# Performance work log

Measured on AMD Instinct MI355X. Metric: run time of the kernel, lower is better.

## Reference

```python
import jax, jax.numpy as jnp
import numpy as np

H_SIZE = 2048
N_HEADS = 16
N_KV = 4
HEAD_DIM = 128
EPS = 1e-6
ROPE_THETA = 10000.0


def _rms_norm(x, w):
    # per-head RMSNorm over last dim (head_dim)
    var = jnp.mean(jnp.square(x), axis=-1, keepdims=True)
    return x * jax.lax.rsqrt(var + EPS) * w


def _rope(x, positions):
    # neox-style rotary over full head_dim. x: [B,S,H,D], positions: [B,S]
    d = x.shape[-1]
    inv_freq = 1.0 / (ROPE_THETA ** (jnp.arange(0, d, 2, dtype=jnp.float32) / d))
    ang = positions.astype(jnp.float32)[..., None] * inv_freq  # [B,S,D/2]
    cos = jnp.cos(ang)[:, :, None, :]
    sin = jnp.sin(ang)[:, :, None, :]
    x1, x2 = x[..., : d // 2], x[..., d // 2 :]
    return jnp.concatenate([x1 * cos - x2 * sin, x2 * cos + x1 * sin], axis=-1)


def setup_inputs() -> dict:
    key = jax.random.key(0)
    k1, k2, k3 = jax.random.split(key, 3)
    B, S = 2, 2048
    positions = jnp.broadcast_to(jnp.arange(S, dtype=jnp.int32), (B, S))
    hidden_states = jax.random.normal(k1, (B, S, H_SIZE), dtype=jnp.float32)
    w_qkv = jax.random.normal(k2, (H_SIZE, (N_HEADS + 2 * N_KV) * HEAD_DIM), dtype=jnp.float32) * 0.02
    w_o = jax.random.normal(k3, (N_HEADS * HEAD_DIM, H_SIZE), dtype=jnp.float32) * 0.02
    q_norm_w = jnp.ones((HEAD_DIM,), dtype=jnp.float32)
    k_norm_w = jnp.ones((HEAD_DIM,), dtype=jnp.float32)
    return {"positions": positions, "hidden_states": hidden_states, "w_qkv": w_qkv,
            "w_o": w_o, "q_norm_w": q_norm_w, "k_norm_w": k_norm_w}


def reference(positions, hidden_states, w_qkv, w_o, q_norm_w, k_norm_w):
    B, S, _ = hidden_states.shape
    q_size = N_HEADS * HEAD_DIM
    kv_size = N_KV * HEAD_DIM
    qkv = hidden_states @ w_qkv  # [B,S,q+2kv]
    q = qkv[..., :q_size].reshape(B, S, N_HEADS, HEAD_DIM)
    k = qkv[..., q_size : q_size + kv_size].reshape(B, S, N_KV, HEAD_DIM)
    v = qkv[..., q_size + kv_size :].reshape(B, S, N_KV, HEAD_DIM)
    q = _rms_norm(q, q_norm_w)
    k = _rms_norm(k, k_norm_w)
    q = _rope(q, positions)
    k = _rope(k, positions)
    # GQA: repeat kv heads
    rep = N_HEADS // N_KV
    k = jnp.repeat(k, rep, axis=2)
    v = jnp.repeat(v, rep, axis=2)
    scale = HEAD_DIM ** -0.5
    scores = jnp.einsum("bqhd,bkhd->bhqk", q, k) * scale
    causal = jnp.tril(jnp.ones((S, S), dtype=bool))
    scores = jnp.where(causal, scores, jnp.finfo(scores.dtype).min)
    probs = jax.nn.softmax(scores, axis=-1)
    attn = jnp.einsum("bhqk,bkhd->bqhd", probs, v).reshape(B, S, N_HEADS * HEAD_DIM)
    return attn @ w_o
```

## Files before the change

### kernel.cpp

```cpp
#include <hip/hip_runtime.h>
#include <math.h>

#define TOKS 4096
#define HS   2048
#define QKV_N 3072
#define S_LEN 2048
#define NH   16
#define NKV  4
#define DH   128

typedef __attribute__((ext_vector_type(8))) short short8;
typedef __attribute__((ext_vector_type(4))) float f32x4;

static __device__ __forceinline__ unsigned short f2bf(float f) {
  unsigned u = __builtin_bit_cast(unsigned, f);
  u += 0x7fffu + ((u >> 16) & 1u);
  return (unsigned short)(u >> 16);
}
static __device__ __forceinline__ float bf2f(unsigned short s) {
  unsigned u = (unsigned)s << 16;
  return __builtin_bit_cast(float, u);
}

__global__ __launch_bounds__(256)
void cvt_bf16(const float* __restrict__ in, unsigned short* __restrict__ out) {
  const size_t i = ((size_t)blockIdx.x * 256 + threadIdx.x) * 8;
  float4 a = *(const float4*)(in + i);
  float4 b = *(const float4*)(in + i + 4);
  short8 r;
  r[0] = f2bf(a.x); r[1] = f2bf(a.y); r[2] = f2bf(a.z); r[3] = f2bf(a.w);
  r[4] = f2bf(b.x); r[5] = f2bf(b.y); r[6] = f2bf(b.z); r[7] = f2bf(b.w);
  *(short8*)(out + i) = r;
}

__global__ __launch_bounds__(256)
void transpose_cvt(const float* __restrict__ in, unsigned short* __restrict__ out,
                   int R, int C, int ldin,
                   long in_z_hi, long in_z_lo, int z_mod, long out_z) {
  __shared__ float tile[32][33];
  const int z = blockIdx.z;
  in  += (size_t)(z / z_mod) * in_z_hi + (size_t)(z % z_mod) * in_z_lo;
  out += (size_t)z * out_z;
  const int r0 = blockIdx.x * 32, c0 = blockIdx.y * 32;
  const int tx = threadIdx.x & 31, ty = threadIdx.x >> 5;
  #pragma unroll
  for (int i = 0; i < 4; ++i)
    tile[ty + i * 8][tx] = in[(size_t)(r0 + ty + i * 8) * ldin + c0 + tx];
  __syncthreads();
  #pragma unroll
  for (int i = 0; i < 4; ++i)
    out[(size_t)(c0 + ty + i * 8) * R + r0 + tx] = f2bf(tile[tx][ty + i * 8]);
}

__global__ __launch_bounds__(256)
void transpose_bf16(const unsigned short* __restrict__ in, unsigned short* __restrict__ out,
                    int R, int C, int ldin,
                    long in_z_hi, long in_z_lo, int z_mod, long out_z) {
  __shared__ unsigned short tile[32][33];
  const int z = blockIdx.z;
  in  += (size_t)(z / z_mod) * in_z_hi + (size_t)(z % z_mod) * in_z_lo;
  out += (size_t)z * out_z;
  const int r0 = blockIdx.x * 32, c0 = blockIdx.y * 32;
  const int tx = threadIdx.x & 31, ty = threadIdx.x >> 5;
  #pragma unroll
  for (int i = 0; i < 4; ++i)
    tile[ty + i * 8][tx] = in[(size_t)(r0 + ty + i * 8) * ldin + c0 + tx];
  __syncthreads();
  #pragma unroll
  for (int i = 0; i < 4; ++i)
    out[(size_t)(c0 + ty + i * 8) * R + r0 + tx] = tile[tx][ty + i * 8];
}

__global__ __launch_bounds__(256)
void norm_rope_cvt(const unsigned short* __restrict__ qkv, const int* __restrict__ positions,
                   const float* __restrict__ qw, const float* __restrict__ kw,
                   unsigned short* __restrict__ Qb, unsigned short* __restrict__ Kb) {
  const int tok  = blockIdx.x;
  const int slot = blockIdx.y * 4 + (threadIdx.x >> 6);
  const int lane = threadIdx.x & 63;
  const int b = tok >> 11, s = tok & 2047;

  const unsigned short* x; const float* wgt; unsigned short* outp; float scale;
  if (slot < NH) {
    x = qkv + (size_t)tok * QKV_N + slot * DH;  wgt = qw;
    outp = Qb + (((size_t)b * NH + slot) * S_LEN + s) * DH;
    scale = 0.08838834764831845f;
  } else {
    const int kh = slot - NH;
    x = qkv + (size_t)tok * QKV_N + NH * DH + kh * DH;  wgt = kw;
    outp = Kb + (((size_t)b * NKV + kh) * S_LEN + s) * DH;
    scale = 1.0f;
  }

  float x1 = bf2f(x[lane]), x2 = bf2f(x[lane + 64]);
  float ss = x1 * x1 + x2 * x2;
  #pragma unroll
  for (int o = 32; o > 0; o >>= 1) ss += __shfl_xor(ss, o, 64);
  const float rs = 1.0f / sqrtf(ss * (1.0f / 128.0f) + 1e-6f);
  const float n1 = x1 * rs * wgt[lane];
  const float n2 = x2 * rs * wgt[lane + 64];

  const float pos = (float)positions[tok];
  const float inv_freq = exp2f(-(float)lane * (13.287712379549449f / 64.0f));
  float sn, cs;
  sincosf(pos * inv_freq, &sn, &cs);

  outp[lane]      = f2bf((n1 * cs - n2 * sn) * scale);
  outp[lane + 64] = f2bf((n2 * cs + n1 * sn) * scale);
}

template <int OUT_BF16, int NB>
__global__ __launch_bounds__(512, 2)
void gemm256(const unsigned short* __restrict__ A, const unsigned short* __restrict__ Bt,
             void* __restrict__ Cv, int M, int N, int K) {
  constexpr int NW   = NB / 4;
  constexpr int NACC = NB / 64;
  constexpr int BL   = NB / 128;
  constexpr int VM   = 2 * BL;

  __shared__ __align__(16) unsigned short LA[2][256 * 64];
  __shared__ __align__(16) unsigned short LB[2][NB * 64];

  const int t = threadIdx.x, w = t >> 6, l = t & 63;
  const int lm = l & 15, lr = l >> 4;
  const int wr = w >> 2, wc = w & 3;
  const int bn = blockIdx.x * NB, bm = blockIdx.y * 256;
  const int nkt = K >> 6;

  f32x4 acc[8][NACC];
  #pragma unroll
  for (int mi = 0; mi < 8; ++mi)
    #pragma unroll
    for (int ni = 0; ni < NACC; ++ni) acc[mi][ni] = {0.f, 0.f, 0.f, 0.f};

  auto stageA = [&](unsigned short* Lb, int half, int kt) {
    if (kt >= nkt) return;
    const int k0 = kt << 6;
    #pragma unroll
    for (int r = 0; r < 2; ++r) {
      const int row  = half * 128 + r * 64 + (t >> 3);
      const int slot = (t & 7) ^ (row & 7);
      const unsigned short* src = A + (size_t)(bm + row) * K + k0 + slot * 8;
      __builtin_amdgcn_global_load_lds(
          (const __attribute__((address_space(1))) void*)src,
          (__attribute__((address_space(3))) void*)(Lb + (half * 128 + r * 64 + w * 8) * 64),
          16, 0, 0);
    }
  };
  auto stageB = [&](unsigned short* Lb, int half, int kt) {
    if (kt >= nkt) return;
    const int k0 = kt << 6;
    #pragma unroll
    for (int r = 0; r < BL; ++r) {
      const int row  = half * (NB / 2) + r * 64 + (t >> 3);
      const int slot = (t & 7) ^ (row & 7);
      const unsigned short* src = Bt + (size_t)(bn + row) * K + k0 + slot * 8;
      __builtin_amdgcn_global_load_lds(
          (const __attribute__((address_space(1))) void*)src,
          (__attribute__((address_space(3))) void*)(Lb + (half * (NB / 2) + r * 64 + w * 8) * 64),
          16, 0, 0);
    }
  };

  stageB(&LB[0][0], 0, 0); stageB(&LB[0][0], 1, 0);
  stageA(&LA[0][0], 0, 0); stageA(&LA[0][0], 1, 0);
  stageB(&LB[1][0], 0, 1); stageB(&LB[1][0], 1, 1);
  if constexpr (NB == 256) asm volatile("s_waitcnt vmcnt(4)" ::: "memory");
  else                     asm volatile("s_waitcnt vmcnt(2)" ::: "memory");
  __builtin_amdgcn_s_barrier();

  const int niter = nkt >> 1;
  for (int i = 0; i < niter; ++i) {
    const int t0 = i * 2;
    short8 bfr[NACC][2];
    #pragma unroll
    for (int p = 0; p < 8; ++p) {
      const int buf = p >> 2, q = p & 3;
      const unsigned short* La = &LA[buf][0];
      const unsigned short* Lb = &LB[buf][0];

      if (q == 0) {
        #pragma unroll
        for (int ni = 0; ni < NACC; ++ni)
          #pragma unroll
          for (int ks = 0; ks < 2; ++ks) {
            const int row = wc * NW + ni * 16 + lm;
            bfr[ni][ks] = *(const short8*)(Lb + row * 64 +
                                           ((ks * 32 + lr * 8) ^ ((row & 7) << 3)));
          }
      }
      short8 af[2][2];
      #pragma unroll
      for (int mi2 = 0; mi2 < 2; ++mi2)
        #pragma unroll
        for (int ks = 0; ks < 2; ++ks) {
          const int row = wr * 128 + (q * 2 + mi2) * 16 + lm;
          af[mi2][ks] = *(const short8*)(La + row * 64 +
                                         ((ks * 32 + lr * 8) ^ ((row & 7) << 3)));
        }

      switch (p) {
        case 0: stageA(&LA[1][0], 0, t0 + 1); break;
        case 1: stageA(&LA[1][0], 1, t0 + 1); break;
        case 2: stageB(&LB[0][0], 0, t0 + 2); break;
        case 3: stageB(&LB[0][0], 1, t0 + 2); break;
        case 4: stageA(&LA[0][0], 0, t0 + 2); break;
        case 5: stageA(&LA[0][0], 1, t0 + 2); break;
        case 6: stageB(&LB[1][0], 0, t0 + 3); break;
        case 7: stageB(&LB[1][0], 1, t0 + 3); break;
      }

      __builtin_amdgcn_s_barrier();
      asm volatile("s_waitcnt lgkmcnt(0)" ::: "memory");
      __builtin_amdgcn_sched_barrier(0);

      __builtin_amdgcn_s_setprio(1);
      #pragma unroll
      for (int mi2 = 0; mi2 < 2; ++mi2)
        #pragma unroll
        for (int ni = 0; ni < NACC; ++ni)
          #pragma unroll
          for (int ks = 0; ks < 2; ++ks)
            acc[q * 2 + mi2][ni] = __builtin_amdgcn_mfma_f32_16x16x32_bf16(
                af[mi2][ks], bfr[ni][ks], acc[q * 2 + mi2][ni], 0, 0, 0);
      __builtin_amdgcn_s_setprio(0);

      if (q == 3) {
        if (i == niter - 1) asm volatile("s_waitcnt vmcnt(0)" ::: "memory");
        else if constexpr (NB == 256) asm volatile("s_waitcnt vmcnt(4)" ::: "memory");
        else                          asm volatile("s_waitcnt vmcnt(2)" ::: "memory");
      }
      __builtin_amdgcn_s_barrier();
    }
  }

  #pragma unroll
  for (int mi = 0; mi < 8; ++mi)
    #pragma unroll
    for (int ni = 0; ni < NACC; ++ni)
      #pragma unroll
      for (int j = 0; j < 4; ++j) {
        const size_t idx =
            (size_t)(bm + wr * 128 + mi * 16 + lr * 4 + j) * N + bn + wc * NW + ni * 16 + lm;
        if constexpr (OUT_BF16) ((unsigned short*)Cv)[idx] = f2bf(acc[mi][ni][j]);
        else                    ((float*)Cv)[idx] = acc[mi][ni][j];
      }
}

#define M_INIT 12.0f
#define P_CAP  2981.0f

__global__ __launch_bounds__(256, 3)
void attn_mfma(const unsigned short* __restrict__ Qb, const unsigned short* __restrict__ Kb,
               const unsigned short* __restrict__ Vt, unsigned short* __restrict__ att) {
  __shared__ unsigned short Ks_[2][64 * 128];
  __shared__ unsigned short Vs_[2][128 * 64];
  __shared__ unsigned short Pl[4][32 * 64];

  const int x  = blockIdx.x;
  const int b  = blockIdx.z;
  const int qb = b ? x : 15 - x;
  const int h  = blockIdx.y;
  const int kvh = h >> 2;
  const int t = threadIdx.x, w = t >> 6, l = t & 63;
  const int lm = l & 15, lr = l >> 4;
  const int row0 = qb * 128 + w * 32;

  const unsigned short* qbase = Qb + ((size_t)(b * NH + h)) * S_LEN * DH;
  const unsigned short* kbase = Kb + ((size_t)(b * NKV + kvh)) * S_LEN * DH;
  const unsigned short* vtbase = Vt + ((size_t)(b * NKV + kvh)) * DH * S_LEN;

  short8 qf[2][4];
  #pragma unroll
  for (int m = 0; m < 2; ++m)
    #pragma unroll
    for (int kc = 0; kc < 4; ++kc)
      qf[m][kc] = *(const short8*)(qbase + (size_t)(row0 + m * 16 + lm) * DH + kc * 32 + lr * 8);

  short8 ones;
  #pragma unroll
  for (int i = 0; i < 8; ++i) ones[i] = (short)0x3F80;

  f32x4 o[2][8];
  #pragma unroll
  for (int m = 0; m < 2; ++m)
    #pragma unroll
    for (int ng = 0; ng < 8; ++ng) o[m][ng] = {0.f, 0.f, 0.f, 0.f};
  f32x4 lacc[2];
  lacc[0] = {0.f, 0.f, 0.f, 0.f}; lacc[1] = {0.f, 0.f, 0.f, 0.f};
  float m_run[2][4];
  #pragma unroll
  for (int m = 0; m < 2; ++m)
    #pragma unroll
    for (int j = 0; j < 4; ++j) m_run[m][j] = M_INIT;

  auto stage = [&](int bufi, int kb0) {
    #pragma unroll
    for (int i = 0; i < 4; ++i) {
      const int rk = w * 16 + i * 4 + (l >> 4);
      const unsigned short* gk =
          kbase + (size_t)(kb0 + rk) * DH + (((l & 15) ^ (rk & 7)) * 8);
      __builtin_amdgcn_global_load_lds(
          (const __attribute__((address_space(1))) void*)gk,
          (__attribute__((address_space(3))) void*)(&Ks_[bufi][(w * 16 + i * 4) * 128]),
          16, 0, 0);
      const int rv = w * 32 + i * 8 + (l >> 3);
      const unsigned short* gv =
          vtbase + (size_t)rv * S_LEN + kb0 + (((l & 7) ^ (rv & 7)) * 8);
      __builtin_amdgcn_global_load_lds(
          (const __attribute__((address_space(1))) void*)gv,
          (__attribute__((address_space(3))) void*)(&Vs_[bufi][(w * 32 + i * 8) * 64]),
          16, 0, 0);
    }
  };

  const int nkt = qb * 2 + 2;
  stage(0, 0);
  __syncthreads();

  for (int kt = 0; kt < nkt; ++kt) {
    const int kb0 = kt * 64;
    if (kt + 1 < nkt) stage((kt + 1) & 1, kb0 + 64);

    if (kb0 <= row0 + 31) {
      const unsigned short* Kc = Ks_[kt & 1];
      const unsigned short* Vc = Vs_[kt & 1];
      const int rsw = (lm & 7) << 3;

      f32x4 s[2][4];
      #pragma unroll
      for (int m = 0; m < 2; ++m)
        #pragma unroll
        for (int n2 = 0; n2 < 4; ++n2) s[m][n2] = {0.f, 0.f, 0.f, 0.f};
      __builtin_amdgcn_s_setprio(1);
      #pragma unroll
      for (int n2 = 0; n2 < 4; ++n2) {
        short8 kf[4];
        #pragma unroll
        for (int kc = 0; kc < 4; ++kc)
          kf[kc] = *(const short8*)(Kc + (n2 * 16 + lm) * 128 + ((kc * 32 + lr * 8) ^ rsw));
        #pragma unroll
        for (int m = 0; m < 2; ++m)
          #pragma unroll
          for (int kc = 0; kc < 4; ++kc)
            s[m][n2] = __builtin_amdgcn_mfma_f32_16x16x32_bf16(qf[m][kc], kf[kc], s[m][n2], 0, 0, 0);
      }
      __builtin_amdgcn_s_setprio(0);

      if (kb0 + 63 > row0) {
        #pragma unroll
        for (int m = 0; m < 2; ++m) {
          const int qi = row0 + m * 16 + lr * 4;
          #pragma unroll
          for (int n2 = 0; n2 < 4; ++n2) {
            const int kvi = kb0 + n2 * 16 + lm;
            #pragma unroll
            for (int j = 0; j < 4; ++j)
              if (kvi > qi + j) s[m][n2][j] = -1e30f;
          }
        }
      }

      float pm = 0.f;
      #pragma unroll
      for (int m = 0; m < 2; ++m)
        #pragma unroll
        for (int n2 = 0; n2 < 4; ++n2)
          #pragma unroll
          for (int j = 0; j < 4; ++j) {
            const float p = __expf(s[m][n2][j] - m_run[m][j]);
            s[m][n2][j] = p;
            pm = fmaxf(pm, p);
          }

      if (!__all(pm <= P_CAP)) {
        #pragma unroll
        for (int m = 0; m < 2; ++m)
          #pragma unroll
          for (int j = 0; j < 4; ++j) {
            float v = fmaxf(fmaxf(s[m][0][j], s[m][1][j]), fmaxf(s[m][2][j], s[m][3][j]));
            v = fmaxf(v, __shfl_xor(v, 1, 64));
            v = fmaxf(v, __shfl_xor(v, 2, 64));
            v = fmaxf(v, __shfl_xor(v, 4, 64));
            v = fmaxf(v, __shfl_xor(v, 8, 64));
            if (v > P_CAP) {
              const float al = 1.0f / v;
              m_run[m][j] += __logf(v);
              lacc[m][j] *= al;
              #pragma unroll
              for (int n2 = 0; n2 < 4; ++n2) s[m][n2][j] *= al;
              #pragma unroll
              for (int ng = 0; ng < 8; ++ng) o[m][ng][j] *= al;
            }
          }
      }

      #pragma unroll
      for (int m = 0; m < 2; ++m)
        #pragma unroll
        for (int j = 0; j < 4; ++j) {
          const int prow = m * 16 + lr * 4 + j;
          unsigned short* Pw = &Pl[w][prow * 64];
          const int sw = (prow & 7) << 3;
          Pw[lm ^ sw]        = f2bf(s[m][0][j]);
          Pw[(16 + lm) ^ sw] = f2bf(s[m][1][j]);
          Pw[(32 + lm) ^ sw] = f2bf(s[m][2][j]);
          Pw[(48 + lm) ^ sw] = f2bf(s[m][3][j]);
        }
      __asm__ volatile("s_waitcnt lgkmcnt(0)" ::: "memory");

      short8 pf[2][2];
      #pragma unroll
      for (int m = 0; m < 2; ++m)
        #pragma unroll
        for (int k2 = 0; k2 < 2; ++k2)
          pf[m][k2] = *(const short8*)(&Pl[w][(m * 16 + lm) * 64 + ((k2 * 32 + lr * 8) ^ rsw)]);
      __builtin_amdgcn_s_setprio(1);
      #pragma unroll
      for (int m = 0; m < 2; ++m)
        #pragma unroll
        for (int k2 = 0; k2 < 2; ++k2)
          lacc[m] = __builtin_amdgcn_mfma_f32_16x16x32_bf16(pf[m][k2], ones, lacc[m], 0, 0, 0);
      #pragma unroll
      for (int ng = 0; ng < 8; ++ng) {
        const short8 vf0 = *(const short8*)(Vc + (ng * 16 + lm) * 64 + ((lr * 8) ^ rsw));
        const short8 vf1 = *(const short8*)(Vc + (ng * 16 + lm) * 64 + ((32 + lr * 8) ^ rsw));
        o[0][ng] = __builtin_amdgcn_mfma_f32_16x16x32_bf16(pf[0][0], vf0, o[0][ng], 0, 0, 0);
        o[1][ng] = __builtin_amdgcn_mfma_f32_16x16x32_bf16(pf[1][0], vf0, o[1][ng], 0, 0, 0);
        o[0][ng] = __builtin_amdgcn_mfma_f32_16x16x32_bf16(pf[0][1], vf1, o[0][ng], 0, 0, 0);
        o[1][ng] = __builtin_amdgcn_mfma_f32_16x16x32_bf16(pf[1][1], vf1, o[1][ng], 0, 0, 0);
      }
      __builtin_amdgcn_s_setprio(0);
    }
    __syncthreads();
  }

  #pragma unroll
  for (int m = 0; m < 2; ++m)
    #pragma unroll
    for (int j = 0; j < 4; ++j) {
      const float linv = 1.0f / lacc[m][j];
      unsigned short* ar =
          att + ((size_t)(b * S_LEN) + row0 + m * 16 + lr * 4 + j) * (NH * DH) + h * DH + lm;
      #pragma unroll
      for (int ng = 0; ng < 8; ++ng) ar[ng * 16] = f2bf(o[m][ng][j] * linv);
    }
}

extern "C" void kernel_launch(void* const* d_in, const int* in_sizes, int n_in,
                              void* d_out, int out_size, void* d_ws, size_t ws_size,
                              hipStream_t stream) {
  const int*   positions = (const int*)  d_in[0];
  const float* hidden    = (const float*)d_in[1];
  const float* w_qkv     = (const float*)d_in[2];
  const float* w_o       = (const float*)d_in[3];
  const float* q_norm_w  = (const float*)d_in[4];
  const float* k_norm_w  = (const float*)d_in[5];
  float* out = (float*)d_out;

  char* ws = (char*)d_ws;
  unsigned short* qkvb  = (unsigned short*)ws;
  unsigned short* att   = (unsigned short*)ws;
  char* region = ws + (size_t)TOKS * QKV_N * 4;
  unsigned short* hb    = (unsigned short*)region;
  unsigned short* Qb    = (unsigned short*)region;
  unsigned short* wqkvt = (unsigned short*)(region + 16777216);
  unsigned short* Kb    = (unsigned short*)(region + 16777216);
  unsigned short* Vt    = (unsigned short*)(region + 20971520);
  unsigned short* wot   = (unsigned short*)(region + 25165824);

  cvt_bf16<<<(TOKS * HS) / (256 * 8), 256, 0, stream>>>(hidden, hb);
  transpose_cvt<<<dim3(HS / 32, QKV_N / 32, 1), 256, 0, stream>>>(
      w_qkv, wqkvt, HS, QKV_N, QKV_N, 0, 0, 1, 0);
  gemm256<1, 256><<<dim3(QKV_N / 256, TOKS / 256), 512, 0, stream>>>(
      hb, wqkvt, qkvb, TOKS, QKV_N, HS);
  norm_rope_cvt<<<dim3(TOKS, 5), 256, 0, stream>>>(
      qkvb, positions, q_norm_w, k_norm_w, Qb, Kb);
  transpose_bf16<<<dim3(S_LEN / 32, DH / 32, 2 * NKV), 256, 0, stream>>>(
      qkvb + (NH + NKV) * DH, Vt, S_LEN, DH, QKV_N,
      (long)S_LEN * QKV_N, DH, NKV, (long)DH * S_LEN);
  transpose_cvt<<<dim3(HS / 32, HS / 32, 1), 256, 0, stream>>>(
      w_o, wot, HS, HS, HS, 0, 0, 1, 0);
  attn_mfma<<<dim3(16, NH, 2), 256, 0, stream>>>(Qb, Kb, Vt, att);
  gemm256<0, 128><<<dim3(HS / 128, TOKS / 256), 512, 0, stream>>>(
      att, wot, out, TOKS, HS, HS);
}
```

Measured before the change: 265.6 us.

## Split long causal attention query blocks across two workgroups with merge kernel

Measured after the change: 270.8 us. No clear change (+2.0%).

```diff
diff --git a/kernel.cpp b/kernel.cpp
--- a/kernel.cpp
+++ b/kernel.cpp
@@ -116,7 +116,6 @@
   constexpr int NW   = NB / 4;
   constexpr int NACC = NB / 64;
   constexpr int BL   = NB / 128;
-  constexpr int VM   = 2 * BL;
 
   __shared__ __align__(16) unsigned short LA[2][256 * 64];
   __shared__ __align__(16) unsigned short LB[2][NB * 64];
@@ -252,18 +251,28 @@
 
 __global__ __launch_bounds__(256, 3)
 void attn_mfma(const unsigned short* __restrict__ Qb, const unsigned short* __restrict__ Kb,
-               const unsigned short* __restrict__ Vt, unsigned short* __restrict__ att) {
+               const unsigned short* __restrict__ Vt, unsigned short* __restrict__ att,
+               float* __restrict__ Opart, float* __restrict__ LMpart) {
   __shared__ unsigned short Ks_[2][64 * 128];
   __shared__ unsigned short Vs_[2][128 * 64];
   __shared__ unsigned short Pl[4][32 * 64];
 
   const int x  = blockIdx.x;
+  const int h  = blockIdx.y;
   const int b  = blockIdx.z;
-  const int qb = b ? x : 15 - x;
-  const int h  = blockIdx.y;
   const int kvh = h >> 2;
   const int t = threadIdx.x, w = t >> 6, l = t & 63;
   const int lm = l & 15, lr = l >> 4;
+
+  int qb, k0t, k1t, pslot;
+  if (x == 0)       { qb = 8; k0t = 0; k1t = 18; pslot = -1; }
+  else if (x <= 14) {
+    const int s = x - 1;  qb = 15 - (s >> 1);
+    const int nk = 2 * qb + 2, mid = nk >> 1, half = s & 1;
+    k0t = half ? mid : 0;  k1t = half ? nk : mid;
+    pslot = ((b * NH + h) * 7 + (qb - 9)) * 2 + half;
+  } else            { qb = 22 - x; k0t = 0; k1t = 2 * qb + 2; pslot = -1; }
+
   const int row0 = qb * 128 + w * 32;
 
   const unsigned short* qbase = Qb + ((size_t)(b * NH + h)) * S_LEN * DH;
@@ -314,13 +323,12 @@
     }
   };
 
-  const int nkt = qb * 2 + 2;
-  stage(0, 0);
+  stage(k0t & 1, k0t * 64);
   __syncthreads();
 
-  for (int kt = 0; kt < nkt; ++kt) {
+  for (int kt = k0t; kt < k1t; ++kt) {
     const int kb0 = kt * 64;
-    if (kt + 1 < nkt) stage((kt + 1) & 1, kb0 + 64);
+    if (kt + 1 < k1t) stage((kt + 1) & 1, kb0 + 64);
 
     if (kb0 <= row0 + 31) {
       const unsigned short* Kc = Ks_[kt & 1];
@@ -435,16 +443,68 @@
     __syncthreads();
   }
 
-  #pragma unroll
-  for (int m = 0; m < 2; ++m)
-    #pragma unroll
-    for (int j = 0; j < 4; ++j) {
-      const float linv = 1.0f / lacc[m][j];
-      unsigned short* ar =
-          att + ((size_t)(b * S_LEN) + row0 + m * 16 + lr * 4 + j) * (NH * DH) + h * DH + lm;
-      #pragma unroll
-      for (int ng = 0; ng < 8; ++ng) ar[ng * 16] = f2bf(o[m][ng][j] * linv);
-    }
+  if (pslot < 0) {
+    #pragma unroll
+    for (int m = 0; m < 2; ++m)
+      #pragma unroll
+      for (int j = 0; j < 4; ++j) {
+        const float linv = 1.0f / lacc[m][j];
+        unsigned short* ar =
+            att + ((size_t)(b * S_LEN) + row0 + m * 16 + lr * 4 + j) * (NH * DH) + h * DH + lm;
+        #pragma unroll
+        for (int ng = 0; ng < 8; ++ng) ar[ng * 16] = f2bf(o[m][ng][j] * linv);
+      }
+  } else {
+    float* Po = Opart + (size_t)pslot * 16384;
+    #pragma unroll
+    for (int m = 0; m < 2; ++m)
+      #pragma unroll
+      for (int j = 0; j < 4; ++j) {
+        const int rl = w * 32 + m * 16 + lr * 4 + j;
+        #pragma unroll
+        for (int ng = 0; ng < 8; ++ng)
+          Po[rl * 128 + ng * 16 + lm] = o[m][ng][j];
+        if (lm == 0) {
+          LMpart[pslot * 256 + rl]       = lacc[m][j];
+          LMpart[pslot * 256 + 128 + rl] = m_run[m][j];
+        }
+      }
+  }
+}
+
+__global__ __launch_bounds__(256)
+void attn_merge(const float* __restrict__ Opart, const float* __restrict__ LMpart,
+                unsigned short* __restrict__ att) {
+  const int qs = blockIdx.x;
+  const int h  = blockIdx.y;
+  const int b  = blockIdx.z;
+  const int qb = 9 + qs;
+  const int sidx = (b * NH + h) * 7 + qs;
+  const int t = threadIdx.x;
+  const int r  = t >> 1;
+  const int c0 = (t & 1) * 64;
+
+  const float l0 = LMpart[(sidx * 2 + 0) * 256 + r];
+  const float m0 = LMpart[(sidx * 2 + 0) * 256 + 128 + r];
+  const float l1 = LMpart[(sidx * 2 + 1) * 256 + r];
+  const float m1 = LMpart[(sidx * 2 + 1) * 256 + 128 + r];
+  const float M  = fmaxf(m0, m1);
+  const float a0 = __expf(m0 - M), a1 = __expf(m1 - M);
+  const float linv = 1.0f / (l0 * a0 + l1 * a1);
+
+  const float* O0 = Opart + ((size_t)(sidx * 2 + 0) * 16384) + r * 128 + c0;
+  const float* O1 = Opart + ((size_t)(sidx * 2 + 1) * 16384) + r * 128 + c0;
+  unsigned short* ar =
+      att + ((size_t)(b * S_LEN) + qb * 128 + r) * (NH * DH) + h * DH + c0;
+  #pragma unroll
+  for (int i = 0; i < 16; ++i) {
+    float4 v0 = *(const float4*)(O0 + i * 4);
+    float4 v1 = *(const float4*)(O1 + i * 4);
+    ar[i * 4 + 0] = f2bf((v0.x * a0 + v1.x * a1) * linv);
+    ar[i * 4 + 1] = f2bf((v0.y * a0 + v1.y * a1) * linv);
+    ar[i * 4 + 2] = f2bf((v0.z * a0 + v1.z * a1) * linv);
+    ar[i * 4 + 3] = f2bf((v0.w * a0 + v1.w * a1) * linv);
+  }
 }
 
 extern "C" void kernel_launch(void* const* d_in, const int* in_sizes, int n_in,
@@ -461,6 +521,8 @@
   char* ws = (char*)d_ws;
   unsigned short* qkvb  = (unsigned short*)ws;
   unsigned short* att   = (unsigned short*)ws;
+  float* Opart  = (float*)(ws + 18874368);
+  float* LMpart = (float*)(ws + 18874368 + 29360128);
   char* region = ws + (size_t)TOKS * QKV_N * 4;
   unsigned short* hb    = (unsigned short*)region;
   unsigned short* Qb    = (unsigned short*)region;
@@ -481,7 +543,8 @@
       (long)S_LEN * QKV_N, DH, NKV, (long)DH * S_LEN);
   transpose_cvt<<<dim3(HS / 32, HS / 32, 1), 256, 0, stream>>>(
       w_o, wot, HS, HS, HS, 0, 0, 1, 0);
-  attn_mfma<<<dim3(16, NH, 2), 256, 0, stream>>>(Qb, Kb, Vt, att);
+  attn_mfma<<<dim3(23, NH, 2), 256, 0, stream>>>(Qb, Kb, Vt, att, Opart, LMpart);
+  attn_merge<<<dim3(7, NH, 2), 256, 0, stream>>>(Opart, LMpart, att);
   gemm256<0, 128><<<dim3(HS / 128, TOKS / 256), 512, 0, stream>>>(
       att, wot, out, TOKS, HS, HS);
 }
```

## Split attention query block across 8 waves of 16 rows each

Applied to the files above, without the earlier changes.

Result: faster. 248.1 us (-6.6%).

```diff
diff --git a/kernel.cpp b/kernel.cpp
--- a/kernel.cpp
+++ b/kernel.cpp
@@ -116,7 +116,6 @@
   constexpr int NW   = NB / 4;
   constexpr int NACC = NB / 64;
   constexpr int BL   = NB / 128;
-  constexpr int VM   = 2 * BL;
 
   __shared__ __align__(16) unsigned short LA[2][256 * 64];
   __shared__ __align__(16) unsigned short LB[2][NB * 64];
@@ -250,12 +249,12 @@
 #define M_INIT 12.0f
 #define P_CAP  2981.0f
 
-__global__ __launch_bounds__(256, 3)
+__global__ __launch_bounds__(512)
 void attn_mfma(const unsigned short* __restrict__ Qb, const unsigned short* __restrict__ Kb,
                const unsigned short* __restrict__ Vt, unsigned short* __restrict__ att) {
   __shared__ unsigned short Ks_[2][64 * 128];
   __shared__ unsigned short Vs_[2][128 * 64];
-  __shared__ unsigned short Pl[4][32 * 64];
+  __shared__ unsigned short Pl[8][16 * 64];
 
   const int x  = blockIdx.x;
   const int b  = blockIdx.z;
@@ -264,52 +263,45 @@
   const int kvh = h >> 2;
   const int t = threadIdx.x, w = t >> 6, l = t & 63;
   const int lm = l & 15, lr = l >> 4;
-  const int row0 = qb * 128 + w * 32;
+  const int row0 = qb * 128 + w * 16;
 
   const unsigned short* qbase = Qb + ((size_t)(b * NH + h)) * S_LEN * DH;
   const unsigned short* kbase = Kb + ((size_t)(b * NKV + kvh)) * S_LEN * DH;
   const unsigned short* vtbase = Vt + ((size_t)(b * NKV + kvh)) * DH * S_LEN;
 
-  short8 qf[2][4];
-  #pragma unroll
-  for (int m = 0; m < 2; ++m)
-    #pragma unroll
-    for (int kc = 0; kc < 4; ++kc)
-      qf[m][kc] = *(const short8*)(qbase + (size_t)(row0 + m * 16 + lm) * DH + kc * 32 + lr * 8);
+  short8 qf[4];
+  #pragma unroll
+  for (int kc = 0; kc < 4; ++kc)
+    qf[kc] = *(const short8*)(qbase + (size_t)(row0 + lm) * DH + kc * 32 + lr * 8);
 
   short8 ones;
   #pragma unroll
   for (int i = 0; i < 8; ++i) ones[i] = (short)0x3F80;
 
-  f32x4 o[2][8];
-  #pragma unroll
-  for (int m = 0; m < 2; ++m)
-    #pragma unroll
-    for (int ng = 0; ng < 8; ++ng) o[m][ng] = {0.f, 0.f, 0.f, 0.f};
-  f32x4 lacc[2];
-  lacc[0] = {0.f, 0.f, 0.f, 0.f}; lacc[1] = {0.f, 0.f, 0.f, 0.f};
-  float m_run[2][4];
-  #pragma unroll
-  for (int m = 0; m < 2; ++m)
-    #pragma unroll
-    for (int j = 0; j < 4; ++j) m_run[m][j] = M_INIT;
+  f32x4 o[8];
+  #pragma unroll
+  for (int ng = 0; ng < 8; ++ng) o[ng] = {0.f, 0.f, 0.f, 0.f};
+  f32x4 lacc = {0.f, 0.f, 0.f, 0.f};
+  float m_run[4];
+  #pragma unroll
+  for (int j = 0; j < 4; ++j) m_run[j] = M_INIT;
 
   auto stage = [&](int bufi, int kb0) {
     #pragma unroll
-    for (int i = 0; i < 4; ++i) {
-      const int rk = w * 16 + i * 4 + (l >> 4);
+    for (int i = 0; i < 2; ++i) {
+      const int rk = i * 32 + w * 4 + (l >> 4);
       const unsigned short* gk =
           kbase + (size_t)(kb0 + rk) * DH + (((l & 15) ^ (rk & 7)) * 8);
       __builtin_amdgcn_global_load_lds(
           (const __attribute__((address_space(1))) void*)gk,
-          (__attribute__((address_space(3))) void*)(&Ks_[bufi][(w * 16 + i * 4) * 128]),
+          (__attribute__((address_space(3))) void*)(&Ks_[bufi][(i * 512 + w * 64) * 8]),
           16, 0, 0);
-      const int rv = w * 32 + i * 8 + (l >> 3);
+      const int rv = i * 64 + w * 8 + (l >> 3);
       const unsigned short* gv =
           vtbase + (size_t)rv * S_LEN + kb0 + (((l & 7) ^ (rv & 7)) * 8);
       __builtin_amdgcn_global_load_lds(
           (const __attribute__((address_space(1))) void*)gv,
-          (__attribute__((address_space(3))) void*)(&Vs_[bufi][(w * 32 + i * 8) * 64]),
+          (__attribute__((address_space(3))) void*)(&Vs_[bufi][(i * 512 + w * 64) * 8]),
           16, 0, 0);
     }
   };
@@ -322,113 +314,92 @@
     const int kb0 = kt * 64;
     if (kt + 1 < nkt) stage((kt + 1) & 1, kb0 + 64);
 
-    if (kb0 <= row0 + 31) {
+    if (kb0 <= row0 + 15) {
       const unsigned short* Kc = Ks_[kt & 1];
       const unsigned short* Vc = Vs_[kt & 1];
       const int rsw = (lm & 7) << 3;
 
-      f32x4 s[2][4];
-      #pragma unroll
-      for (int m = 0; m < 2; ++m)
-        #pragma unroll
-        for (int n2 = 0; n2 < 4; ++n2) s[m][n2] = {0.f, 0.f, 0.f, 0.f};
+      f32x4 s[4];
+      #pragma unroll
+      for (int n2 = 0; n2 < 4; ++n2) s[n2] = {0.f, 0.f, 0.f, 0.f};
       __builtin_amdgcn_s_setprio(1);
       #pragma unroll
       for (int n2 = 0; n2 < 4; ++n2) {
-        short8 kf[4];
-        #pragma unroll
-        for (int kc = 0; kc < 4; ++kc)
-          kf[kc] = *(const short8*)(Kc + (n2 * 16 + lm) * 128 + ((kc * 32 + lr * 8) ^ rsw));
-        #pragma unroll
-        for (int m = 0; m < 2; ++m)
+        #pragma unroll
+        for (int kc = 0; kc < 4; ++kc) {
+          const short8 kf = *(const short8*)(Kc + (n2 * 16 + lm) * 128 +
+                                             ((kc * 32 + lr * 8) ^ rsw));
+          s[n2] = __builtin_amdgcn_mfma_f32_16x16x32_bf16(qf[kc], kf, s[n2], 0, 0, 0);
+        }
+      }
+      __builtin_amdgcn_s_setprio(0);
+
+      if (kb0 + 63 > row0) {
+        const int qi = row0 + lr * 4;
+        #pragma unroll
+        for (int n2 = 0; n2 < 4; ++n2) {
+          const int kvi = kb0 + n2 * 16 + lm;
           #pragma unroll
-          for (int kc = 0; kc < 4; ++kc)
-            s[m][n2] = __builtin_amdgcn_mfma_f32_16x16x32_bf16(qf[m][kc], kf[kc], s[m][n2], 0, 0, 0);
-      }
-      __builtin_amdgcn_s_setprio(0);
-
-      if (kb0 + 63 > row0) {
-        #pragma unroll
-        for (int m = 0; m < 2; ++m) {
-          const int qi = row0 + m * 16 + lr * 4;
-          #pragma unroll
-          for (int n2 = 0; n2 < 4; ++n2) {
-            const int kvi = kb0 + n2 * 16 + lm;
+          for (int j = 0; j < 4; ++j)
+            if (kvi > qi + j) s[n2][j] = -1e30f;
+        }
+      }
+
+      float pm = 0.f;
+      #pragma unroll
+      for (int n2 = 0; n2 < 4; ++n2)
+        #pragma unroll
+        for (int j = 0; j < 4; ++j) {
+          const float p = __expf(s[n2][j] - m_run[j]);
+          s[n2][j] = p;
+          pm = fmaxf(pm, p);
+        }
+
+      if (!__all(pm <= P_CAP)) {
+        #pragma unroll
+        for (int j = 0; j < 4; ++j) {
+          float v = fmaxf(fmaxf(s[0][j], s[1][j]), fmaxf(s[2][j], s[3][j]));
+          v = fmaxf(v, __shfl_xor(v, 1, 64));
+          v = fmaxf(v, __shfl_xor(v, 2, 64));
+          v = fmaxf(v, __shfl_xor(v, 4, 64));
+          v = fmaxf(v, __shfl_xor(v, 8, 64));
+          if (v > P_CAP) {
+            const float al = 1.0f / v;
+            m_run[j] += __logf(v);
+            lacc[j] *= al;
             #pragma unroll
-            for (int j = 0; j < 4; ++j)
-              if (kvi > qi + j) s[m][n2][j] = -1e30f;
+            for (int n2 = 0; n2 < 4; ++n2) s[n2][j] *= al;
+            #pragma unroll
+            for (int ng = 0; ng < 8; ++ng) o[ng][j] *= al;
           }
         }
       }
 
-      float pm = 0.f;
-      #pragma unroll
-      for (int m = 0; m < 2; ++m)
-        #pragma unroll
-        for (int n2 = 0; n2 < 4; ++n2)
-          #pragma unroll
-          for (int j = 0; j < 4; ++j) {
-            const float p = __expf(s[m][n2][j] - m_run[m][j]);
-            s[m][n2][j] = p;
-            pm = fmaxf(pm, p);
-          }
-
-      if (!__all(pm <= P_CAP)) {
-        #pragma unroll
-        for (int m = 0; m < 2; ++m)
-          #pragma unroll
-          for (int j = 0; j < 4; ++j) {
-            float v = fmaxf(fmaxf(s[m][0][j], s[m][1][j]), fmaxf(s[m][2][j], s[m][3][j]));
-            v = fmaxf(v, __shfl_xor(v, 1, 64));
-            v = fmaxf(v, __shfl_xor(v, 2, 64));
-            v = fmaxf(v, __shfl_xor(v, 4, 64));
-            v = fmaxf(v, __shfl_xor(v, 8, 64));
-            if (v > P_CAP) {
-              const float al = 1.0f / v;
-              m_run[m][j] += __logf(v);
-              lacc[m][j] *= al;
-              #pragma unroll
-              for (int n2 = 0; n2 < 4; ++n2) s[m][n2][j] *= al;
-              #pragma unroll
-              for (int ng = 0; ng < 8; ++ng) o[m][ng][j] *= al;
-            }
-          }
-      }
-
-      #pragma unroll
-      for (int m = 0; m < 2; ++m)
-        #pragma unroll
-        for (int j = 0; j < 4; ++j) {
-          const int prow = m * 16 + lr * 4 + j;
-          unsigned short* Pw = &Pl[w][prow * 64];
-          const int sw = (prow & 7) << 3;
-          Pw[lm ^ sw]        = f2bf(s[m][0][j]);
-          Pw[(16 + lm) ^ sw] = f2bf(s[m][1][j]);
-          Pw[(32 + lm) ^ sw] = f2bf(s[m][2][j]);
-          Pw[(48 + lm) ^ sw] = f2bf(s[m][3][j]);
-        }
+      #pragma unroll
+      for (int j = 0; j < 4; ++j) {
+        const int prow = lr * 4 + j;
+        unsigned short* Pw = &Pl[w][prow * 64];
+        const int sw = (prow & 7) << 3;
+        Pw[lm ^ sw]        = f2bf(s[0][j]);
+        Pw[(16 + lm) ^ sw] = f2bf(s[1][j]);
+        Pw[(32 + lm) ^ sw] = f2bf(s[2][j]);
+        Pw[(48 + lm) ^ sw] = f2bf(s[3][j]);
+      }
       __asm__ volatile("s_waitcnt lgkmcnt(0)" ::: "memory");
 
-      short8 pf[2][2];
-      #pragma unroll
-      for (int m = 0; m < 2; ++m)
-        #pragma unroll
-        for (int k2 = 0; k2 < 2; ++k2)
-          pf[m][k2] = *(const short8*)(&Pl[w][(m * 16 + lm) * 64 + ((k2 * 32 + lr * 8) ^ rsw)]);
+      short8 pf[2];
+      #pragma unroll
+      for (int k2 = 0; k2 < 2; ++k2)
+        pf[k2] = *(const short8*)(&Pl[w][lm * 64 + ((k2 * 32 + lr * 8) ^ rsw)]);
       __builtin_amdgcn_s_setprio(1);
-      #pragma unroll
-      for (int m = 0; m < 2; ++m)
-        #pragma unroll
-        for (int k2 = 0; k2 < 2; ++k2)
-          lacc[m] = __builtin_amdgcn_mfma_f32_16x16x32_bf16(pf[m][k2], ones, lacc[m], 0, 0, 0);
+      lacc = __builtin_amdgcn_mfma_f32_16x16x32_bf16(pf[0], ones, lacc, 0, 0, 0);
+      lacc = __builtin_amdgcn_mfma_f32_16x16x32_bf16(pf[1], ones, lacc, 0, 0, 0);
       #pragma unroll
       for (int ng = 0; ng < 8; ++ng) {
         const short8 vf0 = *(const short8*)(Vc + (ng * 16 + lm) * 64 + ((lr * 8) ^ rsw));
         const short8 vf1 = *(const short8*)(Vc + (ng * 16 + lm) * 64 + ((32 + lr * 8) ^ rsw));
-        o[0][ng] = __builtin_amdgcn_mfma_f32_16x16x32_bf16(pf[0][0], vf0, o[0][ng], 0, 0, 0);
-        o[1][ng] = __builtin_amdgcn_mfma_f32_16x16x32_bf16(pf[1][0], vf0, o[1][ng], 0, 0, 0);
-        o[0][ng] = __builtin_amdgcn_mfma_f32_16x16x32_bf16(pf[0][1], vf1, o[0][ng], 0, 0, 0);
-        o[1][ng] = __builtin_amdgcn_mfma_f32_16x16x32_bf16(pf[1][1], vf1, o[1][ng], 0, 0, 0);
+        o[ng] = __builtin_amdgcn_mfma_f32_16x16x32_bf16(pf[0], vf0, o[ng], 0, 0, 0);
+        o[ng] = __builtin_amdgcn_mfma_f32_16x16x32_bf16(pf[1], vf1, o[ng], 0, 0, 0);
       }
       __builtin_amdgcn_s_setprio(0);
     }
@@ -436,15 +407,13 @@
   }
 
   #pragma unroll
-  for (int m = 0; m < 2; ++m)
-    #pragma unroll
-    for (int j = 0; j < 4; ++j) {
-      const float linv = 1.0f / lacc[m][j];
-      unsigned short* ar =
-          att + ((size_t)(b * S_LEN) + row0 + m * 16 + lr * 4 + j) * (NH * DH) + h * DH + lm;
-      #pragma unroll
-      for (int ng = 0; ng < 8; ++ng) ar[ng * 16] = f2bf(o[m][ng][j] * linv);
-    }
+  for (int j = 0; j < 4; ++j) {
+    const float linv = 1.0f / lacc[j];
+    unsigned short* ar =
+        att + ((size_t)(b * S_LEN) + row0 + lr * 4 + j) * (NH * DH) + h * DH + lm;
+    #pragma unroll
+    for (int ng = 0; ng < 8; ++ng) ar[ng * 16] = f2bf(o[ng][j] * linv);
+  }
 }
 
 extern "C" void kernel_launch(void* const* d_in, const int* in_sizes, int n_in,
@@ -481,7 +450,7 @@
       (long)S_LEN * QKV_N, DH, NKV, (long)DH * S_LEN);
   transpose_cvt<<<dim3(HS / 32, HS / 32, 1), 256, 0, stream>>>(
       w_o, wot, HS, HS, HS, 0, 0, 1, 0);
-  attn_mfma<<<dim3(16, NH, 2), 256, 0, stream>>>(Qb, Kb, Vt, att);
+  attn_mfma<<<dim3(16, NH, 2), 512, 0, stream>>>(Qb, Kb, Vt, att);
   gemm256<0, 128><<<dim3(HS / 128, TOKS / 256), 512, 0, stream>>>(
       att, wot, out, TOKS, HS, HS);
 }
```
